# Kernel tuning notes

Hardware: AMD Instinct MI355X
Metric: run time of the kernel (lower is better)

Reference implementation:

```python
import jax, jax.numpy as jnp
import numpy as np
import math

HIDDEN = 768
NUM_HEADS = 12
HEAD_DIM = HIDDEN // NUM_HEADS
MAX_SEQ = 2048
B, S = 4, 1024


def skew_symmetric(v):
    # v: [S,3] -> [S,3,3]
    z = jnp.zeros_like(v[:, 0])
    return jnp.stack([
        jnp.stack([z, -v[:, 2], v[:, 1]], axis=-1),
        jnp.stack([v[:, 2], z, -v[:, 0]], axis=-1),
        jnp.stack([-v[:, 1], v[:, 0], z], axis=-1),
    ], axis=-2)


def se3_exp_map(xi):
    # xi: [S,6] -> R: [S,3,3], t: [S,3]  (faithful to torch so3/se3_exp_map incl. eps clamp)
    omega, v = xi[:, :3], xi[:, 3:]
    theta = jnp.clip(jnp.linalg.norm(omega, axis=1, keepdims=True), 1e-8, None)  # [S,1]
    w = omega / theta
    K = skew_symmetric(w)                       # [S,3,3]
    KK = jnp.matmul(K, K)
    I = jnp.eye(3, dtype=xi.dtype)[None]
    th = theta[:, :, None]                      # [S,1,1]
    st, ct = jnp.sin(th), jnp.cos(th)
    R = I + st * K + (1.0 - ct) * KK
    V = I + (1.0 - ct) / th**2 * K + (th - st) / th**3 * KK
    t = jnp.matmul(V, v[:, :, None])[:, :, 0]   # [S,3]
    return R, t


def setup_inputs() -> dict:
    key = jax.random.key(0)
    ks = jax.random.split(key, 6)
    x = jax.random.normal(ks[0], (B, S, HIDDEN), dtype=jnp.float32)
    # xavier_uniform bound for square [H,H]
    bound = math.sqrt(6.0 / (HIDDEN + HIDDEN))
    Wq = jax.random.uniform(ks[1], (HIDDEN, HIDDEN), minval=-bound, maxval=bound, dtype=jnp.float32)
    Wk = jax.random.uniform(ks[2], (HIDDEN, HIDDEN), minval=-bound, maxval=bound, dtype=jnp.float32)
    Wv = jax.random.uniform(ks[3], (HIDDEN, HIDDEN), minval=-bound, maxval=bound, dtype=jnp.float32)
    Wo = jax.random.uniform(ks[4], (HIDDEN, HIDDEN), minval=-bound, maxval=bound, dtype=jnp.float32)
    rotation_params = jax.random.normal(ks[5], (MAX_SEQ, 6), dtype=jnp.float32) * 0.02
    return {"x": x, "Wq": Wq, "Wk": Wk, "Wv": Wv, "Wo": Wo, "rotation_params": rotation_params}


def _forward(x, Wq, Wk, Wv, Wo, rotation_params):
    b, s, h = x.shape
    nv = h // 3  # hidden_size % 3 == 0, padding branch not taken
    R, t = se3_exp_map(rotation_params[:s])          # [s,3,3], [s,3]
    x3d = x.reshape(b, s, nv, 3)
    xr = jnp.einsum('sij,bsnj->bsni', R, x3d) + t[None, :, None, :]
    xr = xr.reshape(b, s, h)
    # Linear (no bias): y = x @ W.T
    q = jnp.einsum('bsh,oh->bso', xr, Wq).reshape(b, s, NUM_HEADS, HEAD_DIM).transpose(0, 2, 1, 3)
    k = jnp.einsum('bsh,oh->bso', xr, Wk).reshape(b, s, NUM_HEADS, HEAD_DIM).transpose(0, 2, 1, 3)
    v = jnp.einsum('bsh,oh->bso', xr, Wv).reshape(b, s, NUM_HEADS, HEAD_DIM).transpose(0, 2, 1, 3)
    scores = jnp.einsum('bhqd,bhkd->bhqk', q, k) / math.sqrt(HEAD_DIM)
    causal = jnp.tril(jnp.ones((s, s), dtype=bool))
    scores = jnp.where(causal[None, None], scores, -jnp.inf)
    attn = jax.nn.softmax(scores, axis=-1)
    out = jnp.einsum('bhqk,bhkd->bhqd', attn, v).transpose(0, 2, 1, 3).reshape(b, s, h)
    out = jnp.einsum('bsh,oh->bso', out, Wo)
    return out, attn


def reference(x, Wq, Wk, Wv, Wo, rotation_params):
    return _forward(x, Wq, Wk, Wv, Wo, rotation_params)
```

## Files before the change

### kernel.cpp

```cpp
#include <hip/hip_runtime.h>
#include <math.h>

#define S_  1024
#define H_  768
#define NH_ 12
#define HD_ 64
#define BB_ 4

typedef __bf16 bf16x8 __attribute__((ext_vector_type(8)));
typedef float f32x4 __attribute__((ext_vector_type(4)));

__device__ __forceinline__ ushort f2bf(float x) {
    unsigned u = __float_as_uint(x);
    u += 0x7FFF + ((u >> 16) & 1);
    return (ushort)(u >> 16);
}
__device__ __forceinline__ void splitbf(float x, ushort& h, ushort& l) {
    h = f2bf(x);
    float hf = __uint_as_float(((unsigned)h) << 16);
    l = f2bf(x - hf);
}
__device__ __forceinline__ f32x4 mfma16(bf16x8 a, bf16x8 b, f32x4 c) {
    return __builtin_amdgcn_mfma_f32_16x16x32_bf16(a, b, c, 0, 0, 0);
}
#define GLD16(gp, lp) __builtin_amdgcn_global_load_lds( \
    (const __attribute__((address_space(1))) unsigned int*)(gp), \
    (__attribute__((address_space(3))) unsigned int*)(lp), 16, 0, 0)

__device__ __forceinline__ bf16x8 fragld(const ushort* tile, int row, int slot) {
    return *(const bf16x8*)((const char*)tile + row * 128 + ((slot ^ (row & 7)) << 4));
}

__global__ __launch_bounds__(256)
void k_se3(const float* __restrict__ rp, float* __restrict__ Rt) {
    int s = blockIdx.x * 256 + threadIdx.x;
    if (s >= S_) return;
    float wx = rp[s * 6 + 0], wy = rp[s * 6 + 1], wz = rp[s * 6 + 2];
    float vx = rp[s * 6 + 3], vy = rp[s * 6 + 4], vz = rp[s * 6 + 5];
    float th = sqrtf(wx * wx + wy * wy + wz * wz);
    th = fmaxf(th, 1e-8f);
    float inv = 1.0f / th;
    float ux = wx * inv, uy = wy * inv, uz = wz * inv;
    float K[9] = {0.f, -uz, uy,   uz, 0.f, -ux,   -uy, ux, 0.f};
    float KK[9];
    #pragma unroll
    for (int i = 0; i < 3; ++i)
        #pragma unroll
        for (int j = 0; j < 3; ++j) {
            float acc = 0.f;
            #pragma unroll
            for (int k = 0; k < 3; ++k) acc += K[i * 3 + k] * K[k * 3 + j];
            KK[i * 3 + j] = acc;
        }
    float st = sinf(th), ct = cosf(th);
    float omc = 1.0f - ct;
    float c1 = omc / (th * th);
    float c2 = (th - st) / (th * th * th);
    float R[9], V[9];
    #pragma unroll
    for (int i = 0; i < 9; ++i) {
        float I = (i == 0 || i == 4 || i == 8) ? 1.f : 0.f;
        R[i] = I + st * K[i] + omc * KK[i];
        V[i] = I + c1 * K[i] + c2 * KK[i];
    }
    float tx = V[0] * vx + V[1] * vy + V[2] * vz;
    float ty = V[3] * vx + V[4] * vy + V[5] * vz;
    float tz = V[6] * vx + V[7] * vy + V[8] * vz;
    float* o = Rt + s * 12;
    #pragma unroll
    for (int i = 0; i < 9; ++i) o[i] = R[i];
    o[9] = tx; o[10] = ty; o[11] = tz;
}

__global__ __launch_bounds__(256)
void k_rotate_split(const float* __restrict__ x, const float* __restrict__ Rt,
                    ushort* __restrict__ xrh, ushort* __restrict__ xrl) {
    __shared__ float sR[12];
    int bs = blockIdx.x;
    int s = bs & (S_ - 1);
    if (threadIdx.x < 12) sR[threadIdx.x] = Rt[s * 12 + threadIdx.x];
    __syncthreads();
    int v = threadIdx.x;
    const float* xp = x + (size_t)bs * H_ + v * 3;
    float x0 = xp[0], x1 = xp[1], x2 = xp[2];
    float y0 = sR[0] * x0 + sR[1] * x1 + sR[2] * x2 + sR[9];
    float y1 = sR[3] * x0 + sR[4] * x1 + sR[5] * x2 + sR[10];
    float y2 = sR[6] * x0 + sR[7] * x1 + sR[8] * x2 + sR[11];
    size_t o = (size_t)bs * H_ + v * 3;
    ushort h, lo;
    splitbf(y0, h, lo); xrh[o + 0] = h; xrl[o + 0] = lo;
    splitbf(y1, h, lo); xrh[o + 1] = h; xrl[o + 1] = lo;
    splitbf(y2, h, lo); xrh[o + 2] = h; xrl[o + 2] = lo;
}

__global__ __launch_bounds__(256)
void k_wsplit(const float* __restrict__ Wq, const float* __restrict__ Wk,
              const float* __restrict__ Wv, const float* __restrict__ Wo,
              ushort* __restrict__ Wch, ushort* __restrict__ Woh) {
    const int wsel = blockIdx.y;
    const float* src = (wsel == 0) ? Wq : (wsel == 1) ? Wk : (wsel == 2) ? Wv : Wo;
    const int e = (blockIdx.x * 256 + threadIdx.x) * 4;
    float4 xv = *(const float4*)(src + e);
    ushort4 hv = make_ushort4(f2bf(xv.x), f2bf(xv.y), f2bf(xv.z), f2bf(xv.w));
    if (wsel < 3) *(ushort4*)(Wch + (size_t)wsel * (H_ * H_) + e) = hv;
    else          *(ushort4*)(Woh + e) = hv;
}

template<int NF, bool QKV>
__global__ __launch_bounds__(256, 2)
void k_proj2(const ushort* __restrict__ Ah, const ushort* __restrict__ Al,
             const ushort* __restrict__ Bh,
             ushort* __restrict__ qh, ushort* __restrict__ ql,
             ushort* __restrict__ kh, ushort* __restrict__ vh,
             float* __restrict__ outp) {
    constexpr int BN = NF * 32;
    constexpr int TOT = 32 + BN / 8;
    __shared__ __align__(16) ushort sAh[128 * 64];
    __shared__ __align__(16) ushort sAl[128 * 64];
    __shared__ __align__(16) ushort sBh[BN * 64];
    const int mt = blockIdx.x, nt = blockIdx.y;
    const int tid = threadIdx.x, w = tid >> 6, l = tid & 63;
    const int wr = w >> 1, wc = w & 1;
    const int lrow = l >> 3;
    const int ksrc = ((l & 7) ^ lrow) * 8;

    f32x4 acc[4][NF];
    #pragma unroll
    for (int i = 0; i < 4; ++i)
        #pragma unroll
        for (int j = 0; j < NF; ++j) acc[i][j] = (f32x4){0.f, 0.f, 0.f, 0.f};

    for (int kt = 0; kt < H_ / 64; ++kt) {
        const int k0 = kt * 64;
        for (int rr = w; rr < TOT; rr += 4) {
            int t = (rr < 16) ? 0 : (rr < 32) ? 1 : 2;
            int r = rr - ((rr < 16) ? 0 : (rr < 32) ? 16 : 32);
            const ushort* src = (t == 0) ? Ah : (t == 1) ? Al : Bh;
            size_t rowb = (t < 2) ? (size_t)mt * 128 : (size_t)nt * BN;
            const ushort* g = src + (rowb + r * 8 + lrow) * H_ + k0 + ksrc;
            ushort* dstt = (t == 0) ? sAh : (t == 1) ? sAl : sBh;
            GLD16(g, dstt + r * 512);
        }
        __syncthreads();
        #pragma unroll
        for (int ch = 0; ch < 2; ++ch) {
            const int slot = ch * 4 + (l >> 4);
            bf16x8 ah[4], al[4], bh[NF];
            #pragma unroll
            for (int mf = 0; mf < 4; ++mf) {
                int row = wr * 64 + mf * 16 + (l & 15);
                ah[mf] = fragld(sAh, row, slot);
                al[mf] = fragld(sAl, row, slot);
            }
            #pragma unroll
            for (int nf = 0; nf < NF; ++nf)
                bh[nf] = fragld(sBh, wc * (NF * 16) + nf * 16 + (l & 15), slot);
            #pragma unroll
            for (int mf = 0; mf < 4; ++mf)
                #pragma unroll
                for (int nf = 0; nf < NF; ++nf) {
                    acc[mf][nf] = mfma16(ah[mf], bh[nf], acc[mf][nf]);
                    acc[mf][nf] = mfma16(al[mf], bh[nf], acc[mf][nf]);
                }
        }
        __syncthreads();
    }
    #pragma unroll
    for (int mf = 0; mf < 4; ++mf)
        #pragma unroll
        for (int nf = 0; nf < NF; ++nf)
            #pragma unroll
            for (int q = 0; q < 4; ++q) {
                float val = acc[mf][nf][q];
                int row = mt * 128 + wr * 64 + mf * 16 + (l >> 4) * 4 + q;
                int col = nt * BN + wc * (NF * 16) + nf * 16 + (l & 15);
                if constexpr (QKV) {
                    int which = col / H_;
                    int rem = col - which * H_;
                    int hh = rem >> 6, d = rem & 63;
                    int b = row >> 10, s = row & (S_ - 1);
                    if (which == 2) {
                        vh[((size_t)(b * NH_ + hh) * HD_ + d) * S_ + s] = f2bf(val);
                    } else if (which == 1) {
                        kh[(((size_t)(b * NH_ + hh) * S_ + s) << 6) + d] = f2bf(val);
                    } else {
                        size_t idx = (((size_t)(b * NH_ + hh) * S_ + s) << 6) + d;
                        ushort hv, lv; splitbf(val, hv, lv);
                        qh[idx] = hv; ql[idx] = lv;
                    }
                } else {
                    outp[(size_t)row * H_ + col] = val;
                }
            }
}

__global__ __launch_bounds__(256, 2)
void k_scores(const ushort* __restrict__ qh, const ushort* __restrict__ ql,
              const ushort* __restrict__ kh, float* __restrict__ attn) {
    const int mt = blockIdx.x, nt = blockIdx.y, bh = blockIdx.z;
    if (nt > mt) return;
    __shared__ __align__(16) ushort sQh[128 * 64];
    __shared__ __align__(16) ushort sQl[128 * 64];
    __shared__ __align__(16) ushort sKh[128 * 64];
    const int tid = threadIdx.x, w = tid >> 6, l = tid & 63;
    const int wr = w >> 1, wc = w & 1;
    const int lrow = l >> 3, ksrc = ((l & 7) ^ lrow) * 8;
    for (int rr = w; rr < 48; rr += 4) {
        int t = (rr < 16) ? 0 : (rr < 32) ? 1 : 2;
        int r = rr - ((rr < 16) ? 0 : (rr < 32) ? 16 : 32);
        const ushort* src = (t == 0) ? qh : (t == 1) ? ql : kh;
        size_t rowb = (size_t)bh * S_ + (size_t)((t < 2) ? mt : nt) * 128;
        const ushort* g = src + (rowb + r * 8 + lrow) * HD_ + ksrc;
        ushort* dstt = (t == 0) ? sQh : (t == 1) ? sQl : sKh;
        GLD16(g, dstt + r * 512);
    }
    f32x4 acc[4][4];
    #pragma unroll
    for (int i = 0; i < 4; ++i)
        #pragma unroll
        for (int j = 0; j < 4; ++j) acc[i][j] = (f32x4){0.f, 0.f, 0.f, 0.f};
    __syncthreads();
    #pragma unroll
    for (int ch = 0; ch < 2; ++ch) {
        const int slot = ch * 4 + (l >> 4);
        bf16x8 ah[4], al[4], bh4[4];
        #pragma unroll
        for (int mf = 0; mf < 4; ++mf) {
            int row = wr * 64 + mf * 16 + (l & 15);
            ah[mf] = fragld(sQh, row, slot);
            al[mf] = fragld(sQl, row, slot);
        }
        #pragma unroll
        for (int nf = 0; nf < 4; ++nf)
            bh4[nf] = fragld(sKh, wc * 64 + nf * 16 + (l & 15), slot);
        #pragma unroll
        for (int mf = 0; mf < 4; ++mf)
            #pragma unroll
            for (int nf = 0; nf < 4; ++nf) {
                acc[mf][nf] = mfma16(ah[mf], bh4[nf], acc[mf][nf]);
                acc[mf][nf] = mfma16(al[mf], bh4[nf], acc[mf][nf]);
            }
    }
    #pragma unroll
    for (int mf = 0; mf < 4; ++mf)
        #pragma unroll
        for (int nf = 0; nf < 4; ++nf)
            #pragma unroll
            for (int q = 0; q < 4; ++q) {
                int row = mt * 128 + wr * 64 + mf * 16 + (l >> 4) * 4 + q;
                int col = nt * 128 + wc * 64 + nf * 16 + (l & 15);
                attn[((size_t)bh << 20) + ((size_t)row << 10) + col] =
                    acc[mf][nf][q] * 0.125f;
            }
}

__global__ __launch_bounds__(256)
void k_softmax(float* __restrict__ attn) {
    const int q  = blockIdx.x;
    const int bh = blockIdx.y;
    float* row = attn + ((size_t)bh << 20) + ((size_t)q << 10);
    const int tid = threadIdx.x;
    const int j0 = tid * 4;
    __shared__ float redm[4];
    __shared__ float redl[4];
    float4 v = *(const float4*)(row + j0);
    float x0 = (j0 + 0 <= q) ? v.x : -INFINITY;
    float x1 = (j0 + 1 <= q) ? v.y : -INFINITY;
    float x2 = (j0 + 2 <= q) ? v.z : -INFINITY;
    float x3 = (j0 + 3 <= q) ? v.w : -INFINITY;
    float m = fmaxf(fmaxf(x0, x1), fmaxf(x2, x3));
    #pragma unroll
    for (int off = 32; off > 0; off >>= 1) m = fmaxf(m, __shfl_xor(m, off));
    if ((tid & 63) == 0) redm[tid >> 6] = m;
    __syncthreads();
    m = fmaxf(fmaxf(redm[0], redm[1]), fmaxf(redm[2], redm[3]));
    float e0 = __expf(x0 - m), e1 = __expf(x1 - m);
    float e2 = __expf(x2 - m), e3 = __expf(x3 - m);
    float lsum = (e0 + e1) + (e2 + e3);
    #pragma unroll
    for (int off = 32; off > 0; off >>= 1) lsum += __shfl_xor(lsum, off);
    if ((tid & 63) == 0) redl[tid >> 6] = lsum;
    __syncthreads();
    lsum = redl[0] + redl[1] + redl[2] + redl[3];
    float invl = 1.0f / lsum;
    *(float4*)(row + j0) = make_float4(e0 * invl, e1 * invl, e2 * invl, e3 * invl);
}

__global__ __launch_bounds__(256, 2)
void k_pv(const float* __restrict__ attn, const ushort* __restrict__ vh,
          ushort* __restrict__ ctxh, ushort* __restrict__ ctxl) {
    const int mt = blockIdx.x, bh = blockIdx.y;
    __shared__ __align__(16) ushort sPh[128 * 64];
    __shared__ __align__(16) ushort sPl[128 * 64];
    __shared__ __align__(16) ushort sVh[64 * 64];
    const int tid = threadIdx.x, w = tid >> 6, l = tid & 63;
    const int wr = w >> 1, wc = w & 1;
    const int lrow = l >> 3, ksrc = ((l & 7) ^ lrow) * 8;
    f32x4 acc[4][2];
    #pragma unroll
    for (int i = 0; i < 4; ++i)
        #pragma unroll
        for (int j = 0; j < 2; ++j) acc[i][j] = (f32x4){0.f, 0.f, 0.f, 0.f};
    const int nsteps = (mt + 1) * 2;
    for (int kt = 0; kt < nsteps; ++kt) {
        __syncthreads();
        #pragma unroll
        for (int j = 0; j < 8; ++j) {
            int idx = j * 256 + tid;
            int row = idx >> 4, f4 = idx & 15;
            const float* src = attn + ((size_t)bh << 20)
                             + (size_t)(mt * 128 + row) * S_ + kt * 64 + f4 * 4;
            float4 xv = *(const float4*)src;
            ushort h0, h1, h2, h3, l0, l1, l2, l3;
            splitbf(xv.x, h0, l0); splitbf(xv.y, h1, l1);
            splitbf(xv.z, h2, l2); splitbf(xv.w, h3, l3);
            int addr = row * 128 + ((((f4 >> 1) ^ (row & 7))) << 4) + ((f4 & 1) << 3);
            *(ushort4*)((char*)sPh + addr) = make_ushort4(h0, h1, h2, h3);
            *(ushort4*)((char*)sPl + addr) = make_ushort4(l0, l1, l2, l3);
        }
        for (int rr = w; rr < 8; rr += 4) {
            const ushort* g = vh + ((size_t)bh * HD_ + rr * 8 + lrow) * S_
                            + kt * 64 + ksrc;
            GLD16(g, sVh + rr * 512);
        }
        __syncthreads();
        #pragma unroll
        for (int ch = 0; ch < 2; ++ch) {
            const int slot = ch * 4 + (l >> 4);
            bf16x8 ph[4], pl[4], bvh[2];
            #pragma unroll
            for (int mf = 0; mf < 4; ++mf) {
                int row = wr * 64 + mf * 16 + (l & 15);
                ph[mf] = fragld(sPh, row, slot);
                pl[mf] = fragld(sPl, row, slot);
            }
            #pragma unroll
            for (int nf = 0; nf < 2; ++nf)
                bvh[nf] = fragld(sVh, wc * 32 + nf * 16 + (l & 15), slot);
            #pragma unroll
            for (int mf = 0; mf < 4; ++mf)
                #pragma unroll
                for (int nf = 0; nf < 2; ++nf) {
                    acc[mf][nf] = mfma16(ph[mf], bvh[nf], acc[mf][nf]);
                    acc[mf][nf] = mfma16(pl[mf], bvh[nf], acc[mf][nf]);
                }
        }
    }
    const int b = bh / NH_, head = bh - b * NH_;
    #pragma unroll
    for (int mf = 0; mf < 4; ++mf)
        #pragma unroll
        for (int nf = 0; nf < 2; ++nf)
            #pragma unroll
            for (int q = 0; q < 4; ++q) {
                int s = mt * 128 + wr * 64 + mf * 16 + (l >> 4) * 4 + q;
                int d = wc * 32 + nf * 16 + (l & 15);
                size_t idx = ((size_t)(b * S_ + s)) * H_ + head * HD_ + d;
                ushort hv, lv; splitbf(acc[mf][nf][q], hv, lv);
                ctxh[idx] = hv; ctxl[idx] = lv;
            }
}

extern "C" void kernel_launch(void* const* d_in, const int* in_sizes, int n_in,
                              void* d_out, int out_size, void* d_ws, size_t ws_size,
                              hipStream_t stream) {
    (void)in_sizes; (void)n_in; (void)out_size; (void)ws_size;
    const float* x  = (const float*)d_in[0];
    const float* Wq = (const float*)d_in[1];
    const float* Wk = (const float*)d_in[2];
    const float* Wv = (const float*)d_in[3];
    const float* Wo = (const float*)d_in[4];
    const float* rp = (const float*)d_in[5];

    float* out  = (float*)d_out;
    float* attn = out + (size_t)BB_ * S_ * H_;

    char* p = (char*)d_ws;
    auto alloc = [&](size_t bytes) { char* r = p; p += (bytes + 255) & ~(size_t)255; return r; };
    const size_t NE = (size_t)BB_ * S_ * H_;
    float*  Rt   = (float*) alloc(S_ * 12 * 4);
    ushort* xrh  = (ushort*)alloc(NE * 2);
    ushort* xrl  = (ushort*)alloc(NE * 2);
    ushort* Wch  = (ushort*)alloc((size_t)3 * H_ * H_ * 2);
    ushort* Woh  = (ushort*)alloc((size_t)H_ * H_ * 2);
    ushort* qh   = (ushort*)alloc(NE * 2);
    ushort* ql   = (ushort*)alloc(NE * 2);
    ushort* kh   = (ushort*)alloc(NE * 2);
    ushort* vh   = (ushort*)alloc(NE * 2);
    ushort* ctxh = xrh;
    ushort* ctxl = xrl;

    k_se3<<<dim3(4), 256, 0, stream>>>(rp, Rt);
    k_rotate_split<<<dim3(BB_ * S_), 256, 0, stream>>>(x, Rt, xrh, xrl);
    k_wsplit<<<dim3(576, 4), 256, 0, stream>>>(Wq, Wk, Wv, Wo, Wch, Woh);

    k_proj2<4, true><<<dim3(32, 18), 256, 0, stream>>>(
        xrh, xrl, Wch, qh, ql, kh, vh, nullptr);

    k_scores<<<dim3(8, 8, BB_ * NH_), 256, 0, stream>>>(qh, ql, kh, attn);
    k_softmax<<<dim3(S_, BB_ * NH_), 256, 0, stream>>>(attn);
    k_pv<<<dim3(8, BB_ * NH_), 256, 0, stream>>>(attn, vh, ctxh, ctxl);

    k_proj2<2, false><<<dim3(32, 12), 256, 0, stream>>>(
        ctxh, ctxl, Woh, nullptr, nullptr, nullptr, nullptr, out);
}
```

Before: 412.2 us.

## Fuse scores, softmax and PV into two-pass flash-style attention kernels

Replaces the separate scores, softmax and PV kernels with a stats pass that computes per-row online max and inverse sum, followed by a fused kernel. The fused kernel recomputes QK^T, writes normalized probabilities to attn, and multiplies them by V directly from LDS, so the attention matrix is no longer written, reread and rewritten in fp32. In exchange QK^T is computed twice, P is rounded to a single bf16 (no low part) for the PV product, which can reduce accuracy, and the masked upper region is zero-filled explicitly. Causal blocks are unbalanced across the 8x48 grid.

```diff
diff --git a/kernel.cpp b/kernel.cpp
--- a/kernel.cpp
+++ b/kernel.cpp
@@ -195,168 +195,222 @@
 }
 
 __global__ __launch_bounds__(256, 2)
-void k_scores(const ushort* __restrict__ qh, const ushort* __restrict__ ql,
-              const ushort* __restrict__ kh, float* __restrict__ attn) {
-    const int mt = blockIdx.x, nt = blockIdx.y, bh = blockIdx.z;
-    if (nt > mt) return;
-    __shared__ __align__(16) ushort sQh[128 * 64];
-    __shared__ __align__(16) ushort sQl[128 * 64];
-    __shared__ __align__(16) ushort sKh[128 * 64];
+void k_stats(const ushort* __restrict__ qh, const ushort* __restrict__ ql,
+             const ushort* __restrict__ kh, float2* __restrict__ stats) {
+    const int mt = blockIdx.x, bh = blockIdx.y;
+    __shared__ __align__(16) ushort sK[64 * 64];
     const int tid = threadIdx.x, w = tid >> 6, l = tid & 63;
-    const int wr = w >> 1, wc = w & 1;
     const int lrow = l >> 3, ksrc = ((l & 7) ^ lrow) * 8;
-    for (int rr = w; rr < 48; rr += 4) {
-        int t = (rr < 16) ? 0 : (rr < 32) ? 1 : 2;
-        int r = rr - ((rr < 16) ? 0 : (rr < 32) ? 16 : 32);
-        const ushort* src = (t == 0) ? qh : (t == 1) ? ql : kh;
-        size_t rowb = (size_t)bh * S_ + (size_t)((t < 2) ? mt : nt) * 128;
-        const ushort* g = src + (rowb + r * 8 + lrow) * HD_ + ksrc;
-        ushort* dstt = (t == 0) ? sQh : (t == 1) ? sQl : sKh;
-        GLD16(g, dstt + r * 512);
-    }
-    f32x4 acc[4][4];
-    #pragma unroll
-    for (int i = 0; i < 4; ++i)
-        #pragma unroll
-        for (int j = 0; j < 4; ++j) acc[i][j] = (f32x4){0.f, 0.f, 0.f, 0.f};
+    const int qrow = mt * 128 + w * 32;
+    bf16x8 qf[2][2][2];
+    #pragma unroll
+    for (int mf = 0; mf < 2; ++mf)
+        #pragma unroll
+        for (int kc = 0; kc < 2; ++kc) {
+            int row = qrow + mf * 16 + (l & 15);
+            size_t off = (((size_t)bh * S_ + row) << 6) + (kc * 4 + (l >> 4)) * 8;
+            qf[mf][kc][0] = *(const bf16x8*)(qh + off);
+            qf[mf][kc][1] = *(const bf16x8*)(ql + off);
+        }
+    float m_r[2][4], l_r[2][4];
+    #pragma unroll
+    for (int mf = 0; mf < 2; ++mf)
+        #pragma unroll
+        for (int q_ = 0; q_ < 4; ++q_) { m_r[mf][q_] = -INFINITY; l_r[mf][q_] = 0.f; }
+
+    const int nkt = 2 * mt + 2;
+    for (int kt = 0; kt < nkt; ++kt) {
+        __syncthreads();
+        for (int rr = w; rr < 8; rr += 4)
+            GLD16(kh + (((size_t)bh * S_ + kt * 64 + rr * 8 + lrow) << 6) + ksrc,
+                  sK + rr * 512);
+        __syncthreads();
+        f32x4 accs[2][4];
+        #pragma unroll
+        for (int i = 0; i < 2; ++i)
+            #pragma unroll
+            for (int j = 0; j < 4; ++j) accs[i][j] = (f32x4){0.f, 0.f, 0.f, 0.f};
+        #pragma unroll
+        for (int kc = 0; kc < 2; ++kc) {
+            int slot = kc * 4 + (l >> 4);
+            bf16x8 kb[4];
+            #pragma unroll
+            for (int nf = 0; nf < 4; ++nf)
+                kb[nf] = fragld(sK, nf * 16 + (l & 15), slot);
+            #pragma unroll
+            for (int mf = 0; mf < 2; ++mf)
+                #pragma unroll
+                for (int nf = 0; nf < 4; ++nf) {
+                    accs[mf][nf] = mfma16(qf[mf][kc][0], kb[nf], accs[mf][nf]);
+                    accs[mf][nf] = mfma16(qf[mf][kc][1], kb[nf], accs[mf][nf]);
+                }
+        }
+        #pragma unroll
+        for (int mf = 0; mf < 2; ++mf)
+            #pragma unroll
+            for (int q_ = 0; q_ < 4; ++q_) {
+                int R = qrow + mf * 16 + (l >> 4) * 4 + q_;
+                float tmp[4]; float tmax = -INFINITY;
+                #pragma unroll
+                for (int nf = 0; nf < 4; ++nf) {
+                    int j = kt * 64 + nf * 16 + (l & 15);
+                    float xx = accs[mf][nf][q_] * 0.125f;
+                    tmp[nf] = (j <= R) ? xx : -INFINITY;
+                    tmax = fmaxf(tmax, tmp[nf]);
+                }
+                #pragma unroll
+                for (int off = 1; off < 16; off <<= 1)
+                    tmax = fmaxf(tmax, __shfl_xor(tmax, off));
+                float mo = m_r[mf][q_];
+                float mn = fmaxf(mo, tmax);
+                float ts = 0.f;
+                #pragma unroll
+                for (int nf = 0; nf < 4; ++nf) ts += __expf(tmp[nf] - mn);
+                #pragma unroll
+                for (int off = 1; off < 16; off <<= 1) ts += __shfl_xor(ts, off);
+                l_r[mf][q_] = l_r[mf][q_] * __expf(mo - mn) + ts;
+                m_r[mf][q_] = mn;
+            }
+    }
+    if ((l & 15) == 0) {
+        #pragma unroll
+        for (int mf = 0; mf < 2; ++mf)
+            #pragma unroll
+            for (int q_ = 0; q_ < 4; ++q_) {
+                int R = qrow + mf * 16 + (l >> 4) * 4 + q_;
+                stats[(size_t)bh * S_ + R] =
+                    make_float2(m_r[mf][q_], 1.0f / l_r[mf][q_]);
+            }
+    }
+}
+
+__global__ __launch_bounds__(256, 2)
+void k_fused(const ushort* __restrict__ qh, const ushort* __restrict__ ql,
+             const ushort* __restrict__ kh, const ushort* __restrict__ vT,
+             const float2* __restrict__ stats, float* __restrict__ attn,
+             ushort* __restrict__ ctxh, ushort* __restrict__ ctxl) {
+    const int mt = blockIdx.x, bh = blockIdx.y;
+    __shared__ __align__(16) ushort sQP[16384];
+    __shared__ __align__(16) ushort sK[64 * 64];
+    __shared__ __align__(16) ushort sVt[64 * 64];
+    const int tid = threadIdx.x, w = tid >> 6, l = tid & 63;
+    const int lrow = l >> 3, ksrc = ((l & 7) ^ lrow) * 8;
+    const size_t abase = (size_t)bh << 20;
+
+    for (int rr = w; rr < 32; rr += 4) {
+        int t = rr >> 4, r = rr & 15;
+        const ushort* src = t ? ql : qh;
+        GLD16(src + (((size_t)bh * S_ + mt * 128 + r * 8 + lrow) << 6) + ksrc,
+              sQP + t * 8192 + r * 512);
+    }
     __syncthreads();
-    #pragma unroll
-    for (int ch = 0; ch < 2; ++ch) {
-        const int slot = ch * 4 + (l >> 4);
-        bf16x8 ah[4], al[4], bh4[4];
-        #pragma unroll
-        for (int mf = 0; mf < 4; ++mf) {
-            int row = wr * 64 + mf * 16 + (l & 15);
-            ah[mf] = fragld(sQh, row, slot);
-            al[mf] = fragld(sQl, row, slot);
-        }
-        #pragma unroll
-        for (int nf = 0; nf < 4; ++nf)
-            bh4[nf] = fragld(sKh, wc * 64 + nf * 16 + (l & 15), slot);
-        #pragma unroll
-        for (int mf = 0; mf < 4; ++mf)
-            #pragma unroll
-            for (int nf = 0; nf < 4; ++nf) {
-                acc[mf][nf] = mfma16(ah[mf], bh4[nf], acc[mf][nf]);
-                acc[mf][nf] = mfma16(al[mf], bh4[nf], acc[mf][nf]);
-            }
-    }
-    #pragma unroll
-    for (int mf = 0; mf < 4; ++mf)
-        #pragma unroll
-        for (int nf = 0; nf < 4; ++nf)
-            #pragma unroll
-            for (int q = 0; q < 4; ++q) {
-                int row = mt * 128 + wr * 64 + mf * 16 + (l >> 4) * 4 + q;
-                int col = nt * 128 + wc * 64 + nf * 16 + (l & 15);
-                attn[((size_t)bh << 20) + ((size_t)row << 10) + col] =
-                    acc[mf][nf][q] * 0.125f;
-            }
-}
-
-__global__ __launch_bounds__(256)
-void k_softmax(float* __restrict__ attn) {
-    const int q  = blockIdx.x;
-    const int bh = blockIdx.y;
-    float* row = attn + ((size_t)bh << 20) + ((size_t)q << 10);
-    const int tid = threadIdx.x;
-    const int j0 = tid * 4;
-    __shared__ float redm[4];
-    __shared__ float redl[4];
-    float4 v = *(const float4*)(row + j0);
-    float x0 = (j0 + 0 <= q) ? v.x : -INFINITY;
-    float x1 = (j0 + 1 <= q) ? v.y : -INFINITY;
-    float x2 = (j0 + 2 <= q) ? v.z : -INFINITY;
-    float x3 = (j0 + 3 <= q) ? v.w : -INFINITY;
-    float m = fmaxf(fmaxf(x0, x1), fmaxf(x2, x3));
-    #pragma unroll
-    for (int off = 32; off > 0; off >>= 1) m = fmaxf(m, __shfl_xor(m, off));
-    if ((tid & 63) == 0) redm[tid >> 6] = m;
-    __syncthreads();
-    m = fmaxf(fmaxf(redm[0], redm[1]), fmaxf(redm[2], redm[3]));
-    float e0 = __expf(x0 - m), e1 = __expf(x1 - m);
-    float e2 = __expf(x2 - m), e3 = __expf(x3 - m);
-    float lsum = (e0 + e1) + (e2 + e3);
-    #pragma unroll
-    for (int off = 32; off > 0; off >>= 1) lsum += __shfl_xor(lsum, off);
-    if ((tid & 63) == 0) redl[tid >> 6] = lsum;
-    __syncthreads();
-    lsum = redl[0] + redl[1] + redl[2] + redl[3];
-    float invl = 1.0f / lsum;
-    *(float4*)(row + j0) = make_float4(e0 * invl, e1 * invl, e2 * invl, e3 * invl);
-}
-
-__global__ __launch_bounds__(256, 2)
-void k_pv(const float* __restrict__ attn, const ushort* __restrict__ vh,
-          ushort* __restrict__ ctxh, ushort* __restrict__ ctxl) {
-    const int mt = blockIdx.x, bh = blockIdx.y;
-    __shared__ __align__(16) ushort sPh[128 * 64];
-    __shared__ __align__(16) ushort sPl[128 * 64];
-    __shared__ __align__(16) ushort sVh[64 * 64];
-    const int tid = threadIdx.x, w = tid >> 6, l = tid & 63;
-    const int wr = w >> 1, wc = w & 1;
-    const int lrow = l >> 3, ksrc = ((l & 7) ^ lrow) * 8;
-    f32x4 acc[4][2];
-    #pragma unroll
-    for (int i = 0; i < 4; ++i)
-        #pragma unroll
-        for (int j = 0; j < 2; ++j) acc[i][j] = (f32x4){0.f, 0.f, 0.f, 0.f};
-    const int nsteps = (mt + 1) * 2;
-    for (int kt = 0; kt < nsteps; ++kt) {
-        __syncthreads();
-        #pragma unroll
-        for (int j = 0; j < 8; ++j) {
-            int idx = j * 256 + tid;
-            int row = idx >> 4, f4 = idx & 15;
-            const float* src = attn + ((size_t)bh << 20)
-                             + (size_t)(mt * 128 + row) * S_ + kt * 64 + f4 * 4;
-            float4 xv = *(const float4*)src;
-            ushort h0, h1, h2, h3, l0, l1, l2, l3;
-            splitbf(xv.x, h0, l0); splitbf(xv.y, h1, l1);
-            splitbf(xv.z, h2, l2); splitbf(xv.w, h3, l3);
-            int addr = row * 128 + ((((f4 >> 1) ^ (row & 7))) << 4) + ((f4 & 1) << 3);
-            *(ushort4*)((char*)sPh + addr) = make_ushort4(h0, h1, h2, h3);
-            *(ushort4*)((char*)sPl + addr) = make_ushort4(l0, l1, l2, l3);
-        }
-        for (int rr = w; rr < 8; rr += 4) {
-            const ushort* g = vh + ((size_t)bh * HD_ + rr * 8 + lrow) * S_
-                            + kt * 64 + ksrc;
-            GLD16(g, sVh + rr * 512);
-        }
-        __syncthreads();
-        #pragma unroll
-        for (int ch = 0; ch < 2; ++ch) {
-            const int slot = ch * 4 + (l >> 4);
-            bf16x8 ph[4], pl[4], bvh[2];
-            #pragma unroll
-            for (int mf = 0; mf < 4; ++mf) {
-                int row = wr * 64 + mf * 16 + (l & 15);
-                ph[mf] = fragld(sPh, row, slot);
-                pl[mf] = fragld(sPl, row, slot);
-            }
-            #pragma unroll
-            for (int nf = 0; nf < 2; ++nf)
-                bvh[nf] = fragld(sVh, wc * 32 + nf * 16 + (l & 15), slot);
-            #pragma unroll
-            for (int mf = 0; mf < 4; ++mf)
-                #pragma unroll
-                for (int nf = 0; nf < 2; ++nf) {
-                    acc[mf][nf] = mfma16(ph[mf], bvh[nf], acc[mf][nf]);
-                    acc[mf][nf] = mfma16(pl[mf], bvh[nf], acc[mf][nf]);
-                }
-        }
+    bf16x8 qf[2][2][2];
+    #pragma unroll
+    for (int mf = 0; mf < 2; ++mf)
+        #pragma unroll
+        for (int kc = 0; kc < 2; ++kc) {
+            int row = w * 32 + mf * 16 + (l & 15);
+            int slot = kc * 4 + (l >> 4);
+            qf[mf][kc][0] = fragld(sQP, row, slot);
+            qf[mf][kc][1] = fragld(sQP + 8192, row, slot);
+        }
+    float stm[2][4], stl[2][4];
+    #pragma unroll
+    for (int mf = 0; mf < 2; ++mf)
+        #pragma unroll
+        for (int q_ = 0; q_ < 4; ++q_) {
+            int R = mt * 128 + w * 32 + mf * 16 + (l >> 4) * 4 + q_;
+            float2 st = stats[(size_t)bh * S_ + R];
+            stm[mf][q_] = st.x; stl[mf][q_] = st.y;
+        }
+    f32x4 ctx[2][4];
+    #pragma unroll
+    for (int i = 0; i < 2; ++i)
+        #pragma unroll
+        for (int j = 0; j < 4; ++j) ctx[i][j] = (f32x4){0.f, 0.f, 0.f, 0.f};
+    ushort* sPw = sQP + w * 2048;
+
+    const int nkt = 2 * mt + 2;
+    for (int kt = 0; kt < nkt; ++kt) {
+        __syncthreads();
+        for (int rr = w; rr < 8; rr += 4)
+            GLD16(kh + (((size_t)bh * S_ + kt * 64 + rr * 8 + lrow) << 6) + ksrc,
+                  sK + rr * 512);
+        for (int rr = w; rr < 8; rr += 4)
+            GLD16(vT + (((size_t)bh * HD_ + rr * 8 + lrow) << 10) + kt * 64 + ksrc,
+                  sVt + rr * 512);
+        __syncthreads();
+        f32x4 accs[2][4];
+        #pragma unroll
+        for (int i = 0; i < 2; ++i)
+            #pragma unroll
+            for (int j = 0; j < 4; ++j) accs[i][j] = (f32x4){0.f, 0.f, 0.f, 0.f};
+        #pragma unroll
+        for (int kc = 0; kc < 2; ++kc) {
+            int slot = kc * 4 + (l >> 4);
+            bf16x8 kb[4];
+            #pragma unroll
+            for (int nf = 0; nf < 4; ++nf)
+                kb[nf] = fragld(sK, nf * 16 + (l & 15), slot);
+            #pragma unroll
+            for (int mf = 0; mf < 2; ++mf)
+                #pragma unroll
+                for (int nf = 0; nf < 4; ++nf) {
+                    accs[mf][nf] = mfma16(qf[mf][kc][0], kb[nf], accs[mf][nf]);
+                    accs[mf][nf] = mfma16(qf[mf][kc][1], kb[nf], accs[mf][nf]);
+                }
+        }
+        #pragma unroll
+        for (int mf = 0; mf < 2; ++mf)
+            #pragma unroll
+            for (int nf = 0; nf < 4; ++nf)
+                #pragma unroll
+                for (int q_ = 0; q_ < 4; ++q_) {
+                    int rl = mf * 16 + (l >> 4) * 4 + q_;
+                    int R  = mt * 128 + w * 32 + rl;
+                    int j  = kt * 64 + nf * 16 + (l & 15);
+                    float xx = accs[mf][nf][q_] * 0.125f;
+                    float p = (j <= R) ? __expf(xx - stm[mf][q_]) * stl[mf][q_] : 0.f;
+                    attn[abase + ((size_t)R << 10) + j] = p;
+                    int col = nf * 16 + (l & 15);
+                    int a = rl * 128 + ((((col >> 3) ^ (rl & 7))) << 4) + ((col & 7) << 1);
+                    *(ushort*)((char*)sPw + a) = f2bf(p);
+                }
+        #pragma unroll
+        for (int kc = 0; kc < 2; ++kc) {
+            int slot = kc * 4 + (l >> 4);
+            bf16x8 pf[2], vb[4];
+            #pragma unroll
+            for (int mf = 0; mf < 2; ++mf)
+                pf[mf] = fragld(sPw, mf * 16 + (l & 15), slot);
+            #pragma unroll
+            for (int nd = 0; nd < 4; ++nd)
+                vb[nd] = fragld(sVt, nd * 16 + (l & 15), slot);
+            #pragma unroll
+            for (int mf = 0; mf < 2; ++mf)
+                #pragma unroll
+                for (int nd = 0; nd < 4; ++nd)
+                    ctx[mf][nd] = mfma16(pf[mf], vb[nd], ctx[mf][nd]);
+        }
+    }
+    const int c0 = (mt + 1) * 128;
+    const float4 z4 = make_float4(0.f, 0.f, 0.f, 0.f);
+    for (int r = w; r < 128; r += 4) {
+        size_t rb = abase + ((size_t)(mt * 128 + r) << 10);
+        for (int c = c0 + l * 4; c < S_; c += 256)
+            *(float4*)(attn + rb + c) = z4;
     }
     const int b = bh / NH_, head = bh - b * NH_;
     #pragma unroll
-    for (int mf = 0; mf < 4; ++mf)
-        #pragma unroll
-        for (int nf = 0; nf < 2; ++nf)
-            #pragma unroll
-            for (int q = 0; q < 4; ++q) {
-                int s = mt * 128 + wr * 64 + mf * 16 + (l >> 4) * 4 + q;
-                int d = wc * 32 + nf * 16 + (l & 15);
+    for (int mf = 0; mf < 2; ++mf)
+        #pragma unroll
+        for (int nd = 0; nd < 4; ++nd)
+            #pragma unroll
+            for (int q_ = 0; q_ < 4; ++q_) {
+                int s = mt * 128 + w * 32 + mf * 16 + (l >> 4) * 4 + q_;
+                int d = nd * 16 + (l & 15);
                 size_t idx = ((size_t)(b * S_ + s)) * H_ + head * HD_ + d;
-                ushort hv, lv; splitbf(acc[mf][nf][q], hv, lv);
+                ushort hv, lv; splitbf(ctx[mf][nd][q_], hv, lv);
                 ctxh[idx] = hv; ctxl[idx] = lv;
             }
 }
@@ -378,17 +432,18 @@
     char* p = (char*)d_ws;
     auto alloc = [&](size_t bytes) { char* r = p; p += (bytes + 255) & ~(size_t)255; return r; };
     const size_t NE = (size_t)BB_ * S_ * H_;
-    float*  Rt   = (float*) alloc(S_ * 12 * 4);
-    ushort* xrh  = (ushort*)alloc(NE * 2);
-    ushort* xrl  = (ushort*)alloc(NE * 2);
-    ushort* Wch  = (ushort*)alloc((size_t)3 * H_ * H_ * 2);
-    ushort* Woh  = (ushort*)alloc((size_t)H_ * H_ * 2);
-    ushort* qh   = (ushort*)alloc(NE * 2);
-    ushort* ql   = (ushort*)alloc(NE * 2);
-    ushort* kh   = (ushort*)alloc(NE * 2);
-    ushort* vh   = (ushort*)alloc(NE * 2);
-    ushort* ctxh = xrh;
-    ushort* ctxl = xrl;
+    float*  Rt    = (float*) alloc(S_ * 12 * 4);
+    ushort* xrh   = (ushort*)alloc(NE * 2);
+    ushort* xrl   = (ushort*)alloc(NE * 2);
+    ushort* Wch   = (ushort*)alloc((size_t)3 * H_ * H_ * 2);
+    ushort* Woh   = (ushort*)alloc((size_t)H_ * H_ * 2);
+    ushort* qh    = (ushort*)alloc(NE * 2);
+    ushort* ql    = (ushort*)alloc(NE * 2);
+    ushort* kh    = (ushort*)alloc(NE * 2);
+    ushort* vh    = (ushort*)alloc(NE * 2);
+    float2* stats = (float2*)alloc((size_t)BB_ * NH_ * S_ * 8);
+    ushort* ctxh  = xrh;
+    ushort* ctxl  = xrl;
 
     k_se3<<<dim3(4), 256, 0, stream>>>(rp, Rt);
     k_rotate_split<<<dim3(BB_ * S_), 256, 0, stream>>>(x, Rt, xrh, xrl);
@@ -397,9 +452,9 @@
     k_proj2<4, true><<<dim3(32, 18), 256, 0, stream>>>(
         xrh, xrl, Wch, qh, ql, kh, vh, nullptr);
 
-    k_scores<<<dim3(8, 8, BB_ * NH_), 256, 0, stream>>>(qh, ql, kh, attn);
-    k_softmax<<<dim3(S_, BB_ * NH_), 256, 0, stream>>>(attn);
-    k_pv<<<dim3(8, BB_ * NH_), 256, 0, stream>>>(attn, vh, ctxh, ctxl);
+    k_stats<<<dim3(8, BB_ * NH_), 256, 0, stream>>>(qh, ql, kh, stats);
+    k_fused<<<dim3(8, BB_ * NH_), 256, 0, stream>>>(qh, ql, kh, vh, stats,
+                                                    attn, ctxh, ctxl);
 
     k_proj2<2, false><<<dim3(32, 12), 256, 0, stream>>>(
         ctxh, ctxl, Woh, nullptr, nullptr, nullptr, nullptr, out);
```

After: 394.9 us. 1.04x faster.
